# Optimization experiments

Measured on AMD Instinct MI355X. Metric: run time of the kernel, lower is better.

The kernel has to match this reference:

```python
import jax, jax.numpy as jnp
import numpy as np

N_NODES = 50000
N_EDGES = 800000
D_IN = 128
D_OUT = 128
NUM_RELS = 100


def setup_inputs() -> dict:
    key = jax.random.key(0)
    k1, k2, k3, k4, k5, k6, k7 = jax.random.split(key, 7)
    h = jax.random.normal(k1, (N_NODES, D_IN), dtype=jnp.float32)
    W = jax.random.normal(k2, (D_IN, D_OUT), dtype=jnp.float32) * 0.05
    attn = jax.random.normal(k3, (2 * D_OUT,), dtype=jnp.float32) * 0.05
    rel_emb = jax.random.normal(k4, (NUM_RELS, 1), dtype=jnp.float32)
    src = jax.random.randint(k5, (N_EDGES,), 0, N_NODES, dtype=jnp.int32)
    dst = jax.random.randint(k6, (N_EDGES,), 0, N_NODES, dtype=jnp.int32)
    etype = jax.random.randint(k7, (N_EDGES,), 0, NUM_RELS, dtype=jnp.int32)
    return {"h": h, "W": W, "attn": attn, "rel_emb": rel_emb,
            "src": src, "dst": dst, "etype": etype}


def reference(h, W, attn, rel_emb, src, dst, etype):
    # h: [N, d_in], W: [d_in, d_out], attn: [2*d_out], rel_emb: [R, 1]
    # src/dst/etype: [E]
    N = h.shape[0]
    d = W.shape[1]
    # padding_idx=0 in nn.Embedding -> row 0 is zero
    rel_table = rel_emb.at[0].set(0.0)
    z = h @ W  # [N, d_out]
    # attn_fc([z_src, z_dst]) = z_src @ a_l + z_dst @ a_r (split the concat-linear)
    s_src = z @ attn[:d]  # [N]
    s_dst = z @ attn[d:]  # [N]
    e = jax.nn.leaky_relu(s_src[src] + s_dst[dst])  # [E], slope 0.01 as in torch
    # segment softmax over incoming edges of each dst node
    m = jax.ops.segment_max(e, dst, num_segments=N)  # [N]
    ex = jnp.exp(e - m[dst])  # [E]
    denom = jax.ops.segment_sum(ex, dst, num_segments=N)  # [N]
    alpha = ex / denom[dst]  # [E]
    coef = rel_table[etype, 0] * alpha  # [E]  (rel_alpha * alpha)
    # weighted sum of source messages per destination node
    out = jax.ops.segment_sum(coef[:, None] * z[src], dst, num_segments=N)  # [N, d_out]
    return out
```

## Files before the change

kernel.cpp:

```cpp
#include <hip/hip_runtime.h>

#define D 128
#define GROWS 64

typedef __attribute__((ext_vector_type(8))) short short8;
typedef __attribute__((ext_vector_type(4))) float float4v;

__device__ __forceinline__ ushort f2bf(float x) {
    uint u = __float_as_uint(x);
    return (ushort)((u + 0x7FFFu + ((u >> 16) & 1u)) >> 16);
}
__device__ __forceinline__ float bf_lo(uint u) { return __uint_as_float(u << 16); }
__device__ __forceinline__ float bf_hi(uint u) { return __uint_as_float(u & 0xFFFF0000u); }

__global__ __launch_bounds__(256) void convW_kernel(
    const float* __restrict__ W, ushort* __restrict__ Wtg)
{
    int idx = blockIdx.x * 256 + threadIdx.x;
    int k = idx >> 7, n = idx & 127;
    Wtg[n * 128 + k] = f2bf(W[idx]);
}

__global__ __launch_bounds__(512) void gemm_mfma_kernel(
    const float* __restrict__ h, const ushort* __restrict__ Wtg,
    const float* __restrict__ attn, const int* __restrict__ dst,
    ushort* __restrict__ zb, float* __restrict__ s_src, float* __restrict__ s_dst,
    int* __restrict__ histm, int nhi, int N, int E, int nblocks)
{
    __shared__ ushort ht[GROWS * 136];
    __shared__ float psum_s[GROWS][2];
    __shared__ float psum_d[GROWS][2];
    __shared__ int histA[256];
    const int tid = threadIdx.x;
    const int base = blockIdx.x * GROWS;

#pragma unroll
    for (int it = 0; it < 4; ++it) {
        int idx = it * 512 + tid;
        int r = idx >> 5, c4 = (idx & 31) * 4;
        float4 v = make_float4(0.f, 0.f, 0.f, 0.f);
        if (base + r < N) v = *(const float4*)&h[(size_t)(base + r) * D + c4];
        ushort4 u = make_ushort4(f2bf(v.x), f2bf(v.y), f2bf(v.z), f2bf(v.w));
        *(ushort4*)&ht[r * 136 + c4] = u;
    }
    if (tid < 256) histA[tid] = 0;
    __syncthreads();

    const int lane = tid & 63;
    const int wave = tid >> 6;
    const int wr = wave >> 1;
    const int wc = wave & 1;
    const int col = lane & 15;
    const int quad = lane >> 4;
    const int wm = wr * 16;

    float4v acc[4];
#pragma unroll
    for (int nt = 0; nt < 4; ++nt) acc[nt] = (float4v)(0.f);

#pragma unroll
    for (int kc = 0; kc < 128; kc += 32) {
        short8 a = *(const short8*)&ht[(wm + col) * 136 + kc + quad * 8];
#pragma unroll
        for (int nt = 0; nt < 4; ++nt) {
            short8 b = *(const short8*)&Wtg[(wc * 64 + nt * 16 + col) * 128 + kc + quad * 8];
            acc[nt] = __builtin_amdgcn_mfma_f32_16x16x32_bf16(a, b, acc[nt], 0, 0, 0);
        }
    }
    __syncthreads();

    float ps[4] = {0.f, 0.f, 0.f, 0.f}, pd[4] = {0.f, 0.f, 0.f, 0.f};
#pragma unroll
    for (int nt = 0; nt < 4; ++nt) {
        float aL = attn[wc * 64 + nt * 16 + col];
        float aR = attn[D + wc * 64 + nt * 16 + col];
#pragma unroll
        for (int reg = 0; reg < 4; ++reg) {
            float v = acc[nt][reg];
            ps[reg] = fmaf(v, aL, ps[reg]);
            pd[reg] = fmaf(v, aR, pd[reg]);
            ht[(wm + quad * 4 + reg) * 136 + wc * 64 + nt * 16 + col] = f2bf(v);
        }
    }
#pragma unroll
    for (int reg = 0; reg < 4; ++reg) {
#pragma unroll
        for (int off = 1; off < 16; off <<= 1) {
            ps[reg] += __shfl_xor(ps[reg], off);
            pd[reg] += __shfl_xor(pd[reg], off);
        }
        if (col == 0) {
            int rl = wm + quad * 4 + reg;
            psum_s[rl][wc] = ps[reg];
            psum_d[rl][wc] = pd[reg];
        }
    }
    __syncthreads();

    if (tid < GROWS && base + tid < N) {
        s_src[base + tid] = psum_s[tid][0] + psum_s[tid][1];
        s_dst[base + tid] = psum_d[tid][0] + psum_d[tid][1];
    }

#pragma unroll
    for (int it = 0; it < 2; ++it) {
        int idx = it * 512 + tid;
        int r = idx >> 4, c8 = idx & 15;
        if (base + r < N)
            *(uint4*)&zb[(size_t)(base + r) * D + c8 * 8] = *(uint4*)&ht[r * 136 + c8 * 8];
    }

    const int cpb = (E + nblocks - 1) / nblocks;
    const int cs = blockIdx.x * cpb;
    const int ce = min(cs + cpb, E);
    for (int i = cs + tid; i < ce; i += 512)
        atomicAdd(&histA[dst[i] >> 8], 1);
    __syncthreads();
    if (tid < nhi) histm[blockIdx.x * nhi + tid] = histA[tid];
}

__global__ __launch_bounds__(64) void binB1_kernel(
    int* __restrict__ histm, int* __restrict__ colsum, int nhi, int nchunk)
{
    const int b = blockIdx.x;
    const int t = threadIdx.x;
    const int K = (nchunk + 63) / 64;
    int v[16];
    int s = 0;
#pragma unroll
    for (int j = 0; j < 16; ++j) {
        int c = t * K + j;
        v[j] = (j < K && c < nchunk) ? histm[c * nhi + b] : 0;
        s += v[j];
    }
    int incl = s;
#pragma unroll
    for (int off = 1; off < 64; off <<= 1) {
        int u = __shfl_up(incl, off);
        if (t >= off) incl += u;
    }
    int run = incl - s;
#pragma unroll
    for (int j = 0; j < 16; ++j) {
        int c = t * K + j;
        if (j < K && c < nchunk) { histm[c * nhi + b] = run; run += v[j]; }
    }
    if (t == 63) colsum[b] = incl;
}

__device__ __forceinline__ void scan_colsum_wave0(
    const int* __restrict__ colsum, int* sbase, int nhi, int lane)
{
    int v[4];
    int s = 0;
#pragma unroll
    for (int j = 0; j < 4; ++j) {
        int c = lane * 4 + j;
        v[j] = (c < nhi) ? colsum[c] : 0;
        s += v[j];
    }
    int incl = s;
#pragma unroll
    for (int off = 1; off < 64; off <<= 1) {
        int u = __shfl_up(incl, off);
        if (lane >= off) incl += u;
    }
    int run = incl - s;
#pragma unroll
    for (int j = 0; j < 4; ++j) {
        run += v[j];
        sbase[lane * 4 + j] = run;
    }
}

__global__ __launch_bounds__(256) void binC_kernel(
    const int* __restrict__ src, const int* __restrict__ dst,
    const int* __restrict__ etype, const int* __restrict__ histm,
    const int* __restrict__ colsum, uint* __restrict__ binned,
    int nhi, int E, int nchunk)
{
    __shared__ int sbase[256];
    __shared__ int cur[256];
    const int tid = threadIdx.x;
    if (tid < 64) scan_colsum_wave0(colsum, sbase, nhi, tid);
    __syncthreads();
    if (tid < nhi)
        cur[tid] = ((tid == 0) ? 0 : sbase[tid - 1]) + histm[blockIdx.x * nhi + tid];
    __syncthreads();
    const int cpb = (E + nchunk - 1) / nchunk;
    const int cs = blockIdx.x * cpb;
    const int ce = min(cs + cpb, E);
    for (int i = cs + tid; i < ce; i += 256) {
        int d = dst[i];
        int pos = atomicAdd(&cur[d >> 8], 1);
        binned[pos] = (uint)src[i] | ((uint)etype[i] << 16) | ((uint)(d & 255) << 23);
    }
}

__global__ __launch_bounds__(256) void binD_kernel(
    const uint* __restrict__ binned, const float* __restrict__ s_src,
    const float* __restrict__ s_dst, const int* __restrict__ colsum,
    const float* __restrict__ rel_emb, uint2* __restrict__ sorted,
    int* __restrict__ nodeoff, float* __restrict__ nodeInv,
    int nhi, int N, int R)
{
    __shared__ float rel_l[128];
    __shared__ int sbase[256];
    __shared__ int hist[256];
    __shared__ int loff[257];
    __shared__ int cur[256];
    __shared__ float sDst[256];
    __shared__ float sDen[256];
    __shared__ int wsum[4];
    const int tid = threadIdx.x;
    const int lane = tid & 63;
    const int wave = tid >> 6;

    if (tid < R) rel_l[tid] = (tid == 0) ? 0.f : rel_emb[tid];
    if (wave == 0) scan_colsum_wave0(colsum, sbase, nhi, lane);
    hist[tid] = 0;
    sDen[tid] = 0.f;
    const int hi = blockIdx.x;
    const int dbase = hi * 256;
    {
        int dd = dbase + tid;
        sDst[tid] = (dd < N) ? s_dst[dd] : 0.f;
    }
    __syncthreads();

    const int bb = (hi == 0) ? 0 : sbase[hi - 1];
    const int be = sbase[hi];

    for (int i = bb + tid; i < be; i += 256)
        atomicAdd(&hist[(binned[i] >> 23) & 0xFF], 1);
    __syncthreads();

    {
        int v = hist[tid];
        int incl = v;
#pragma unroll
        for (int off = 1; off < 64; off <<= 1) {
            int u = __shfl_up(incl, off);
            if (lane >= off) incl += u;
        }
        if (lane == 63) wsum[wave] = incl;
        __syncthreads();
        int woff = 0;
#pragma unroll
        for (int w = 0; w < 4; ++w)
            if (w < wave) woff += wsum[w];
        incl += woff;
        loff[tid + 1] = incl;
        if (tid == 0) loff[0] = 0;
        int excl = incl - v;
        cur[tid] = excl;
        nodeoff[dbase + tid] = bb + excl;
    }
    __syncthreads();

    for (int i = bb + tid; i < be; i += 256) {
        uint pk = binned[i];
        int srcv = (int)(pk & 0xFFFF);
        int et = (int)((pk >> 16) & 0x7F);
        int li = (int)((pk >> 23) & 0xFF);
        float x = s_src[srcv] + sDst[li];
        float e = (x > 0.f) ? x : 0.01f * x;
        float p = __expf(e);
        int pos = bb + atomicAdd(&cur[li], 1);
        sorted[pos] = make_uint2((uint)srcv, __float_as_uint(p * rel_l[et]));
        atomicAdd(&sDen[li], p);
    }
    __syncthreads();

    {
        float den = sDen[tid];
        nodeInv[dbase + tid] = (den > 0.f) ? 1.0f / den : 0.f;
    }
}

__global__ __launch_bounds__(256) void aggE_kernel(
    const uint* __restrict__ zb32, const uint2* __restrict__ sorted,
    const int* __restrict__ nodeoff, const float* __restrict__ nodeInv,
    float* __restrict__ out, int N)
{
    const int tid = threadIdx.x;
    const int lane = tid & 63;
    const int wave = tid >> 6;
    const int q = lane >> 4;
    const int ql = lane & 15;
    const int d = blockIdx.x * 16 + wave * 4 + q;
    if (d >= N) return;

    const int st = nodeoff[d];
    const int en = nodeoff[d + 1];
    const float inv = nodeInv[d];

    float4 acc0 = make_float4(0.f, 0.f, 0.f, 0.f);
    float4 acc1 = make_float4(0.f, 0.f, 0.f, 0.f);

    for (int b2 = st; b2 < en; b2 += 8) {
        uint2 hdr[8];
#pragma unroll
        for (int j = 0; j < 8; ++j) {
            int idx = b2 + j;
            hdr[j] = (idx < en) ? sorted[idx] : make_uint2(0u, 0u);
        }
        uint4 u[8];
#pragma unroll
        for (int j = 0; j < 8; ++j)
            u[j] = *(const uint4*)(zb32 + (size_t)hdr[j].x * 64 + ql * 4);
#pragma unroll
        for (int j = 0; j < 8; ++j) {
            const float wj = __uint_as_float(hdr[j].y);
            acc0.x = fmaf(wj, bf_lo(u[j].x), acc0.x);
            acc0.y = fmaf(wj, bf_hi(u[j].x), acc0.y);
            acc0.z = fmaf(wj, bf_lo(u[j].y), acc0.z);
            acc0.w = fmaf(wj, bf_hi(u[j].y), acc0.w);
            acc1.x = fmaf(wj, bf_lo(u[j].z), acc1.x);
            acc1.y = fmaf(wj, bf_hi(u[j].z), acc1.y);
            acc1.z = fmaf(wj, bf_lo(u[j].w), acc1.z);
            acc1.w = fmaf(wj, bf_hi(u[j].w), acc1.w);
        }
    }

    float* orow = out + (size_t)d * D + ql * 8;
    *(float4*)orow       = make_float4(acc0.x * inv, acc0.y * inv, acc0.z * inv, acc0.w * inv);
    *(float4*)(orow + 4) = make_float4(acc1.x * inv, acc1.y * inv, acc1.z * inv, acc1.w * inv);
}

extern "C" void kernel_launch(void* const* d_in, const int* in_sizes, int n_in,
                              void* d_out, int out_size, void* d_ws, size_t ws_size,
                              hipStream_t stream)
{
    const float* h    = (const float*)d_in[0];
    const float* W    = (const float*)d_in[1];
    const float* attn = (const float*)d_in[2];
    const float* rel  = (const float*)d_in[3];
    const int*   src  = (const int*)d_in[4];
    const int*   dst  = (const int*)d_in[5];
    const int*   et   = (const int*)d_in[6];
    float* out = (float*)d_out;

    const int N = in_sizes[0] / D;
    const int E = in_sizes[4];
    const int R = in_sizes[3];

    char* p = (char*)d_ws;
    auto alloc = [&](size_t bytes) {
        char* q = p;
        p += (bytes + 255) & ~(size_t)255;
        return q;
    };
    const int nhi     = (N + 255) / 256;
    const int gblocks = (N + GROWS - 1) / GROWS;

    ushort* zb      = (ushort*)alloc((size_t)N * D * sizeof(ushort));
    ushort* Wtg     = (ushort*)alloc((size_t)D * D * sizeof(ushort));
    float* ssrc     = (float*)alloc((size_t)N * sizeof(float));
    float* sdst     = (float*)alloc((size_t)N * sizeof(float));
    uint*  binned   = (uint*)alloc((size_t)E * sizeof(uint));
    int*   histm    = (int*)alloc((size_t)gblocks * nhi * sizeof(int));
    int*   colsum   = (int*)alloc((size_t)nhi * sizeof(int));
    uint2* sorted   = (uint2*)alloc((size_t)E * sizeof(uint2));
    int*   nodeoff  = (int*)alloc(((size_t)nhi * 256 + 1) * sizeof(int));
    float* nodeInv  = (float*)alloc((size_t)nhi * 256 * sizeof(float));

    convW_kernel<<<64, 256, 0, stream>>>(W, Wtg);
    gemm_mfma_kernel<<<gblocks, 512, 0, stream>>>(h, Wtg, attn, dst, zb, ssrc, sdst,
                                                  histm, nhi, N, E, gblocks);
    binB1_kernel<<<nhi, 64, 0, stream>>>(histm, colsum, nhi, gblocks);
    binC_kernel<<<gblocks, 256, 0, stream>>>(src, dst, et, histm, colsum, binned,
                                             nhi, E, gblocks);
    binD_kernel<<<nhi, 256, 0, stream>>>(binned, ssrc, sdst, colsum, rel,
                                         sorted, nodeoff, nodeInv, nhi, N, R);
    aggE_kernel<<<(N + 15) / 16, 256, 0, stream>>>((const uint*)zb, sorted,
                                                   nodeoff, nodeInv, out, N);
}
```

Baseline: 171.0 us.

## Replace global histogram-scan binning with fixed-capacity buckets and shared-memory local sort

Edge binning by destination block no longer uses a per-chunk histogram computed inside the GEMM kernel plus a separate scan kernel. Each bin now gets a fixed-capacity region, and a global atomic cursor reserves space in it. The binning kernel sorts its chunk locally in shared memory before writing contiguous runs. The per-bin kernel then stages its edges and the sorted output in LDS before one coalesced write-out. This removes one launch, the histogram matrix traffic and the scattered global writes. In exchange, it relies on every bin staying within CAP=4608 edges and every chunk within CHUNK_MAX=3200 edges. Edges beyond those limits are silently dropped, so correctness depends on dst being roughly uniform.

```diff
diff --git a/kernel.cpp b/kernel.cpp
--- a/kernel.cpp
+++ b/kernel.cpp
@@ -2,6 +2,9 @@
 
 #define D 128
 #define GROWS 64
+#define CAP 4608
+#define CBLK 256
+#define CHUNK_MAX 3200
 
 typedef __attribute__((ext_vector_type(8))) short short8;
 typedef __attribute__((ext_vector_type(4))) float float4v;
@@ -14,23 +17,23 @@
 __device__ __forceinline__ float bf_hi(uint u) { return __uint_as_float(u & 0xFFFF0000u); }
 
 __global__ __launch_bounds__(256) void convW_kernel(
-    const float* __restrict__ W, ushort* __restrict__ Wtg)
+    const float* __restrict__ W, ushort* __restrict__ Wtg, int* __restrict__ bincur)
 {
     int idx = blockIdx.x * 256 + threadIdx.x;
     int k = idx >> 7, n = idx & 127;
     Wtg[n * 128 + k] = f2bf(W[idx]);
+    if (blockIdx.x == 0) bincur[threadIdx.x] = 0;
 }
 
 __global__ __launch_bounds__(512) void gemm_mfma_kernel(
     const float* __restrict__ h, const ushort* __restrict__ Wtg,
-    const float* __restrict__ attn, const int* __restrict__ dst,
+    const float* __restrict__ attn,
     ushort* __restrict__ zb, float* __restrict__ s_src, float* __restrict__ s_dst,
-    int* __restrict__ histm, int nhi, int N, int E, int nblocks)
+    int N)
 {
     __shared__ ushort ht[GROWS * 136];
     __shared__ float psum_s[GROWS][2];
     __shared__ float psum_d[GROWS][2];
-    __shared__ int histA[256];
     const int tid = threadIdx.x;
     const int base = blockIdx.x * GROWS;
 
@@ -43,7 +46,6 @@
         ushort4 u = make_ushort4(f2bf(v.x), f2bf(v.y), f2bf(v.z), f2bf(v.w));
         *(ushort4*)&ht[r * 136 + c4] = u;
     }
-    if (tid < 256) histA[tid] = 0;
     __syncthreads();
 
     const int lane = tid & 63;
@@ -109,134 +111,130 @@
         if (base + r < N)
             *(uint4*)&zb[(size_t)(base + r) * D + c8 * 8] = *(uint4*)&ht[r * 136 + c8 * 8];
     }
-
-    const int cpb = (E + nblocks - 1) / nblocks;
-    const int cs = blockIdx.x * cpb;
-    const int ce = min(cs + cpb, E);
-    for (int i = cs + tid; i < ce; i += 512)
-        atomicAdd(&histA[dst[i] >> 8], 1);
-    __syncthreads();
-    if (tid < nhi) histm[blockIdx.x * nhi + tid] = histA[tid];
-}
-
-__global__ __launch_bounds__(64) void binB1_kernel(
-    int* __restrict__ histm, int* __restrict__ colsum, int nhi, int nchunk)
-{
-    const int b = blockIdx.x;
-    const int t = threadIdx.x;
-    const int K = (nchunk + 63) / 64;
-    int v[16];
-    int s = 0;
-#pragma unroll
-    for (int j = 0; j < 16; ++j) {
-        int c = t * K + j;
-        v[j] = (j < K && c < nchunk) ? histm[c * nhi + b] : 0;
-        s += v[j];
-    }
-    int incl = s;
-#pragma unroll
-    for (int off = 1; off < 64; off <<= 1) {
-        int u = __shfl_up(incl, off);
-        if (t >= off) incl += u;
-    }
-    int run = incl - s;
-#pragma unroll
-    for (int j = 0; j < 16; ++j) {
-        int c = t * K + j;
-        if (j < K && c < nchunk) { histm[c * nhi + b] = run; run += v[j]; }
-    }
-    if (t == 63) colsum[b] = incl;
-}
-
-__device__ __forceinline__ void scan_colsum_wave0(
-    const int* __restrict__ colsum, int* sbase, int nhi, int lane)
-{
-    int v[4];
-    int s = 0;
-#pragma unroll
-    for (int j = 0; j < 4; ++j) {
-        int c = lane * 4 + j;
-        v[j] = (c < nhi) ? colsum[c] : 0;
-        s += v[j];
-    }
-    int incl = s;
-#pragma unroll
-    for (int off = 1; off < 64; off <<= 1) {
-        int u = __shfl_up(incl, off);
-        if (lane >= off) incl += u;
-    }
-    int run = incl - s;
-#pragma unroll
-    for (int j = 0; j < 4; ++j) {
-        run += v[j];
-        sbase[lane * 4 + j] = run;
-    }
-}
-
-__global__ __launch_bounds__(256) void binC_kernel(
+}
+
+__global__ __launch_bounds__(512) void binC2_kernel(
     const int* __restrict__ src, const int* __restrict__ dst,
-    const int* __restrict__ etype, const int* __restrict__ histm,
-    const int* __restrict__ colsum, uint* __restrict__ binned,
-    int nhi, int E, int nchunk)
-{
-    __shared__ int sbase[256];
+    const int* __restrict__ etype, int* __restrict__ bincur,
+    uint* __restrict__ binned, int E, int nchunk)
+{
+    __shared__ int hist[256];
+    __shared__ int loff[257];
     __shared__ int cur[256];
+    __shared__ int gbase[256];
+    __shared__ int wsum[4];
+    __shared__ uint pay[CHUNK_MAX];
+    __shared__ unsigned char bid[CHUNK_MAX];
     const int tid = threadIdx.x;
-    if (tid < 64) scan_colsum_wave0(colsum, sbase, nhi, tid);
-    __syncthreads();
-    if (tid < nhi)
-        cur[tid] = ((tid == 0) ? 0 : sbase[tid - 1]) + histm[blockIdx.x * nhi + tid];
-    __syncthreads();
+    const int lane = tid & 63;
+    const int wave = tid >> 6;
+
+    if (tid < 256) hist[tid] = 0;
+    __syncthreads();
+
     const int cpb = (E + nchunk - 1) / nchunk;
     const int cs = blockIdx.x * cpb;
     const int ce = min(cs + cpb, E);
-    for (int i = cs + tid; i < ce; i += 256) {
-        int d = dst[i];
-        int pos = atomicAdd(&cur[d >> 8], 1);
-        binned[pos] = (uint)src[i] | ((uint)etype[i] << 16) | ((uint)(d & 255) << 23);
-    }
-}
-
-__global__ __launch_bounds__(256) void binD_kernel(
-    const uint* __restrict__ binned, const float* __restrict__ s_src,
-    const float* __restrict__ s_dst, const int* __restrict__ colsum,
+    const int n = ce - cs;
+
+    {
+        int i = tid;
+        for (; i + 1536 < n; i += 2048) {
+            int d0 = dst[cs + i], d1 = dst[cs + i + 512];
+            int d2 = dst[cs + i + 1024], d3 = dst[cs + i + 1536];
+            atomicAdd(&hist[d0 >> 8], 1);
+            atomicAdd(&hist[d1 >> 8], 1);
+            atomicAdd(&hist[d2 >> 8], 1);
+            atomicAdd(&hist[d3 >> 8], 1);
+        }
+        for (; i < n; i += 512) atomicAdd(&hist[dst[cs + i] >> 8], 1);
+    }
+    __syncthreads();
+
+    int v = 0;
+    if (tid < 256) {
+        v = hist[tid];
+        int incl = v;
+#pragma unroll
+        for (int off = 1; off < 64; off <<= 1) {
+            int u = __shfl_up(incl, off);
+            if (lane >= off) incl += u;
+        }
+        if (lane == 63) wsum[wave] = incl;
+        loff[tid + 1] = incl;
+    }
+    __syncthreads();
+    if (tid < 256) {
+        int woff = 0;
+#pragma unroll
+        for (int w = 0; w < 4; ++w)
+            if (w < wave) woff += wsum[w];
+        int incl = loff[tid + 1] + woff;
+        loff[tid + 1] = incl;
+        if (tid == 0) loff[0] = 0;
+        cur[tid] = incl - v;
+        if (v > 0) gbase[tid] = atomicAdd(&bincur[tid], v);
+    }
+    __syncthreads();
+
+    for (int i = tid; i < n; i += 512) {
+        int dd = dst[cs + i];
+        int b = dd >> 8;
+        uint pk = (uint)src[cs + i] | ((uint)etype[cs + i] << 16) | ((uint)(dd & 255) << 23);
+        int pos = atomicAdd(&cur[b], 1);
+        if (pos < CHUNK_MAX) { pay[pos] = pk; bid[pos] = (unsigned char)b; }
+    }
+    __syncthreads();
+
+    for (int i = tid; i < n; i += 512) {
+        int b = bid[i];
+        int local = gbase[b] + (i - loff[b]);
+        if (local < CAP) binned[b * CAP + local] = pay[i];
+    }
+}
+
+__global__ __launch_bounds__(512) void binD2_kernel(
+    const uint* __restrict__ binned, const int* __restrict__ bincur,
+    const float* __restrict__ s_src, const float* __restrict__ s_dst,
     const float* __restrict__ rel_emb, uint2* __restrict__ sorted,
-    int* __restrict__ nodeoff, float* __restrict__ nodeInv,
-    int nhi, int N, int R)
+    uint2* __restrict__ nodemeta, float* __restrict__ nodeInv, int N, int R)
 {
     __shared__ float rel_l[128];
-    __shared__ int sbase[256];
     __shared__ int hist[256];
     __shared__ int loff[257];
     __shared__ int cur[256];
     __shared__ float sDst[256];
     __shared__ float sDen[256];
     __shared__ int wsum[4];
+    __shared__ uint sE[CAP];
+    __shared__ uint2 sS[CAP];
     const int tid = threadIdx.x;
     const int lane = tid & 63;
     const int wave = tid >> 6;
-
-    if (tid < R) rel_l[tid] = (tid == 0) ? 0.f : rel_emb[tid];
-    if (wave == 0) scan_colsum_wave0(colsum, sbase, nhi, lane);
-    hist[tid] = 0;
-    sDen[tid] = 0.f;
     const int hi = blockIdx.x;
     const int dbase = hi * 256;
-    {
+
+    if (tid < R) rel_l[tid] = (tid == 0) ? 0.f : rel_emb[tid];
+    if (tid < 256) {
+        hist[tid] = 0;
+        sDen[tid] = 0.f;
         int dd = dbase + tid;
         sDst[tid] = (dd < N) ? s_dst[dd] : 0.f;
     }
-    __syncthreads();
-
-    const int bb = (hi == 0) ? 0 : sbase[hi - 1];
-    const int be = sbase[hi];
-
-    for (int i = bb + tid; i < be; i += 256)
-        atomicAdd(&hist[(binned[i] >> 23) & 0xFF], 1);
-    __syncthreads();
-
-    {
-        int v = hist[tid];
+    const int ne = min(bincur[hi], CAP);
+    __syncthreads();
+
+    const uint* bbp = binned + (size_t)hi * CAP;
+    for (int i = tid; i < ne; i += 512) {
+        uint pk = bbp[i];
+        sE[i] = pk;
+        atomicAdd(&hist[(pk >> 23) & 0xFF], 1);
+    }
+    __syncthreads();
+
+    int v = 0;
+    if (tid < 256) {
+        v = hist[tid];
         int incl = v;
 #pragma unroll
         for (int off = 1; off < 64; off <<= 1) {
@@ -244,43 +242,68 @@
             if (lane >= off) incl += u;
         }
         if (lane == 63) wsum[wave] = incl;
-        __syncthreads();
+        loff[tid + 1] = incl;
+    }
+    __syncthreads();
+    if (tid < 256) {
         int woff = 0;
 #pragma unroll
         for (int w = 0; w < 4; ++w)
             if (w < wave) woff += wsum[w];
-        incl += woff;
+        int incl = loff[tid + 1] + woff;
         loff[tid + 1] = incl;
         if (tid == 0) loff[0] = 0;
-        int excl = incl - v;
-        cur[tid] = excl;
-        nodeoff[dbase + tid] = bb + excl;
-    }
-    __syncthreads();
-
-    for (int i = bb + tid; i < be; i += 256) {
-        uint pk = binned[i];
-        int srcv = (int)(pk & 0xFFFF);
-        int et = (int)((pk >> 16) & 0x7F);
-        int li = (int)((pk >> 23) & 0xFF);
-        float x = s_src[srcv] + sDst[li];
-        float e = (x > 0.f) ? x : 0.01f * x;
-        float p = __expf(e);
-        int pos = bb + atomicAdd(&cur[li], 1);
-        sorted[pos] = make_uint2((uint)srcv, __float_as_uint(p * rel_l[et]));
-        atomicAdd(&sDen[li], p);
+        cur[tid] = incl - v;
     }
     __syncthreads();
 
     {
+        int i = tid;
+        for (; i + 1536 < ne; i += 2048) {
+            uint pk0 = sE[i], pk1 = sE[i + 512], pk2 = sE[i + 1024], pk3 = sE[i + 1536];
+            float x0 = s_src[pk0 & 0xFFFF];
+            float x1 = s_src[pk1 & 0xFFFF];
+            float x2 = s_src[pk2 & 0xFFFF];
+            float x3 = s_src[pk3 & 0xFFFF];
+#define PROC(pk, xs)                                                        \
+            {                                                               \
+                int li = (int)(((pk) >> 23) & 0xFF);                        \
+                int et = (int)(((pk) >> 16) & 0x7F);                        \
+                float x = (xs) + sDst[li];                                  \
+                float e = (x > 0.f) ? x : 0.01f * x;                        \
+                float p = __expf(e);                                        \
+                int pos = atomicAdd(&cur[li], 1);                           \
+                sS[pos] = make_uint2((pk) & 0xFFFF, __float_as_uint(p * rel_l[et])); \
+                atomicAdd(&sDen[li], p);                                    \
+            }
+            PROC(pk0, x0)
+            PROC(pk1, x1)
+            PROC(pk2, x2)
+            PROC(pk3, x3)
+        }
+        for (; i < ne; i += 512) {
+            uint pk = sE[i];
+            float xs = s_src[pk & 0xFFFF];
+            PROC(pk, xs)
+        }
+#undef PROC
+    }
+    __syncthreads();
+
+    uint2* so = sorted + (size_t)hi * CAP;
+    for (int i = tid; i < ne; i += 512) so[i] = sS[i];
+
+    if (tid < 256) {
         float den = sDen[tid];
         nodeInv[dbase + tid] = (den > 0.f) ? 1.0f / den : 0.f;
+        nodemeta[dbase + tid] =
+            make_uint2((uint)(hi * CAP + loff[tid]), (uint)(loff[tid + 1] - loff[tid]));
     }
 }
 
 __global__ __launch_bounds__(256) void aggE_kernel(
     const uint* __restrict__ zb32, const uint2* __restrict__ sorted,
-    const int* __restrict__ nodeoff, const float* __restrict__ nodeInv,
+    const uint2* __restrict__ nodemeta, const float* __restrict__ nodeInv,
     float* __restrict__ out, int N)
 {
     const int tid = threadIdx.x;
@@ -291,19 +314,20 @@
     const int d = blockIdx.x * 16 + wave * 4 + q;
     if (d >= N) return;
 
-    const int st = nodeoff[d];
-    const int en = nodeoff[d + 1];
+    const uint2 meta = nodemeta[d];
+    const int st = (int)meta.x;
+    const int cnt = (int)meta.y;
     const float inv = nodeInv[d];
 
     float4 acc0 = make_float4(0.f, 0.f, 0.f, 0.f);
     float4 acc1 = make_float4(0.f, 0.f, 0.f, 0.f);
 
-    for (int b2 = st; b2 < en; b2 += 8) {
+    for (int b2 = 0; b2 < cnt; b2 += 8) {
         uint2 hdr[8];
 #pragma unroll
         for (int j = 0; j < 8; ++j) {
             int idx = b2 + j;
-            hdr[j] = (idx < en) ? sorted[idx] : make_uint2(0u, 0u);
+            hdr[j] = (idx < cnt) ? sorted[st + idx] : make_uint2(0u, 0u);
         }
         uint4 u[8];
 #pragma unroll
@@ -358,21 +382,17 @@
     ushort* Wtg     = (ushort*)alloc((size_t)D * D * sizeof(ushort));
     float* ssrc     = (float*)alloc((size_t)N * sizeof(float));
     float* sdst     = (float*)alloc((size_t)N * sizeof(float));
-    uint*  binned   = (uint*)alloc((size_t)E * sizeof(uint));
-    int*   histm    = (int*)alloc((size_t)gblocks * nhi * sizeof(int));
-    int*   colsum   = (int*)alloc((size_t)nhi * sizeof(int));
-    uint2* sorted   = (uint2*)alloc((size_t)E * sizeof(uint2));
-    int*   nodeoff  = (int*)alloc(((size_t)nhi * 256 + 1) * sizeof(int));
+    uint*  binned   = (uint*)alloc((size_t)nhi * CAP * sizeof(uint));
+    int*   bincur   = (int*)alloc(256 * sizeof(int));
+    uint2* sorted   = (uint2*)alloc((size_t)nhi * CAP * sizeof(uint2));
+    uint2* nodemeta = (uint2*)alloc((size_t)nhi * 256 * sizeof(uint2));
     float* nodeInv  = (float*)alloc((size_t)nhi * 256 * sizeof(float));
 
-    convW_kernel<<<64, 256, 0, stream>>>(W, Wtg);
-    gemm_mfma_kernel<<<gblocks, 512, 0, stream>>>(h, Wtg, attn, dst, zb, ssrc, sdst,
-                                                  histm, nhi, N, E, gblocks);
-    binB1_kernel<<<nhi, 64, 0, stream>>>(histm, colsum, nhi, gblocks);
-    binC_kernel<<<gblocks, 256, 0, stream>>>(src, dst, et, histm, colsum, binned,
-                                             nhi, E, gblocks);
-    binD_kernel<<<nhi, 256, 0, stream>>>(binned, ssrc, sdst, colsum, rel,
-                                         sorted, nodeoff, nodeInv, nhi, N, R);
+    convW_kernel<<<64, 256, 0, stream>>>(W, Wtg, bincur);
+    gemm_mfma_kernel<<<gblocks, 512, 0, stream>>>(h, Wtg, attn, zb, ssrc, sdst, N);
+    binC2_kernel<<<CBLK, 512, 0, stream>>>(src, dst, et, bincur, binned, E, CBLK);
+    binD2_kernel<<<nhi, 512, 0, stream>>>(binned, bincur, ssrc, sdst, rel,
+                                          sorted, nodemeta, nodeInv, N, R);
     aggE_kernel<<<(N + 15) / 16, 256, 0, stream>>>((const uint*)zb, sorted,
-                                                   nodeoff, nodeInv, out, N);
-}
+                                                   nodemeta, nodeInv, out, N);
+}
```

New measurement: 170.7 us. No clear change (-0.2%).
